# Optimization experiments

Hardware: AMD Instinct MI355X
Metric: run time of the kernel (lower is better)

## Reference

```python
import jax, jax.numpy as jnp
import numpy as np

B, T, D, H = 256, 128, 76, 128  # batch, time, features, lstm hidden (bidirectional -> 2H states)


def setup_inputs() -> dict:
    key = jax.random.key(0)
    ks = jax.random.split(key, 30)
    u = lambda k, shape: jax.random.uniform(k, shape, jnp.float32, -0.1, 0.1)
    inp = {}
    inp['x'] = jax.random.normal(ks[0], (B, T, D), jnp.float32)
    inp['eps_z'] = jax.random.normal(ks[1], (2, B, H), jnp.float32)
    inp['eps_on'] = jax.random.normal(ks[2], (B, T, 2 * H), jnp.float32)
    # encoder/decoder bidirectional LSTM weights: [dir, 4H, in] / [dir, 4H, H] / [dir, 4H]
    inp['enc_Wih'] = u(ks[3], (2, 4 * H, D)); inp['enc_Whh'] = u(ks[4], (2, 4 * H, H)); inp['enc_b'] = u(ks[5], (2, 4 * H))
    inp['dec_Wih'] = u(ks[6], (2, 4 * H, D)); inp['dec_Whh'] = u(ks[7], (2, 4 * H, H)); inp['dec_b'] = u(ks[8], (2, 4 * H))
    inp['Wzmu'] = u(ks[9], (H, H)); inp['bzmu'] = u(ks[10], (H,))
    inp['Wzlv'] = u(ks[11], (H, H)); inp['bzlv'] = u(ks[12], (H,))
    inp['Womu'] = u(ks[13], (2 * H, 2 * H)); inp['bomu'] = u(ks[14], (2 * H,))
    inp['Wolv'] = u(ks[15], (2 * H, 2 * H)); inp['bolv'] = u(ks[16], (2 * H,))
    inp['att_v'] = u(ks[17], (2 * H,))
    inp['att_W1'] = u(ks[18], (2 * H, 2 * H)); inp['att_b1'] = u(ks[19], (2 * H,))
    inp['att_W2'] = u(ks[20], (2 * H, 2 * H)); inp['att_b2'] = u(ks[21], (2 * H,))
    inp['Wout'] = u(ks[22], (D, 4 * H)); inp['bout'] = u(ks[23], (D,))
    return inp


def lstm_cell(xt, h, c, Wih, Whh, b):
    # PyTorch gate order: i, f, g, o
    g = xt @ Wih.T + h @ Whh.T + b
    i, f, gg, o = jnp.split(g, 4, axis=-1)
    c = jax.nn.sigmoid(f) * c + jax.nn.sigmoid(i) * jnp.tanh(gg)
    h = jax.nn.sigmoid(o) * jnp.tanh(c)
    return h, c


def reference(x, eps_z, eps_on, enc_Wih, enc_Whh, enc_b, dec_Wih, dec_Whh, dec_b,
              Wzmu, bzmu, Wzlv, bzlv, Womu, bomu, Wolv, bolv,
              att_v, att_W1, att_b1, att_W2, att_b2, Wout, bout):
    Bx, Tx, Dx = x.shape
    Hx = enc_Whh.shape[-1]
    xT = jnp.swapaxes(x, 0, 1)  # [T,B,D]
    h0 = jnp.zeros((Bx, Hx), x.dtype)
    c0 = jnp.zeros((Bx, Hx), x.dtype)

    def enc_step(d):
        def step(carry, xt):
            h, c = carry
            h, c = lstm_cell(xt, h, c, enc_Wih[d], enc_Whh[d], enc_b[d])
            return (h, c), h
        return step

    (hf, _), out_f = jax.lax.scan(enc_step(0), (h0, c0), xT)
    (hb, _), out_b = jax.lax.scan(enc_step(1), (h0, c0), xT[::-1])
    on = jnp.swapaxes(jnp.concatenate([out_f, out_b[::-1]], axis=-1), 0, 1)  # [B,T,2H]
    hn = jnp.stack([hf, hb])  # [2,B,H]

    # VAE reparameterization on final hidden and on encoder outputs
    mu_z = hn @ Wzmu.T + bzmu
    logvar_z = hn @ Wzlv.T + bzlv
    z = mu_z + eps_z * jnp.exp(0.5 * logvar_z)  # [2,B,H]
    mu_on = on @ Womu.T + bomu
    logvar_on = on @ Wolv.T + bolv
    on_s = mu_on + eps_on * jnp.exp(0.5 * logvar_on)  # [B,T,2H]

    # attention key projection precomputed once (W_2(values))
    W2v = on_s @ att_W2.T + att_b2  # [B,T,2H]
    # teacher forcing (prob=1.0): step t input is zeros at t=0, x[:,t-1] after
    dec_in = jnp.concatenate([jnp.zeros((1, Bx, Dx), x.dtype), xT[:-1]], axis=0)  # [T,B,D]

    def dec_step(carry, inp_t):
        h, c = carry  # each [2,B,H]
        q = jnp.concatenate([h[0], h[1]], axis=1)  # [B,2H]
        scores = jnp.tanh((q @ att_W1.T + att_b1)[:, None, :] + W2v) @ att_v  # [B,T]
        w = jax.nn.softmax(scores, axis=1)
        # (weights.unsqueeze(2) * values).mean(dim=1) -> weighted sum / T
        ctx = jnp.einsum('bt,btd->bd', w, on_s) / Tx  # [B,2H]
        h0n, c0n = lstm_cell(inp_t, h[0], c[0], dec_Wih[0], dec_Whh[0], dec_b[0])
        h1n, c1n = lstm_cell(inp_t, h[1], c[1], dec_Wih[1], dec_Whh[1], dec_b[1])
        out = jnp.concatenate([h0n, h1n, ctx], axis=1) @ Wout.T + bout  # [B,D]
        return (jnp.stack([h0n, h1n]), jnp.stack([c0n, c1n])), out

    _, outs = jax.lax.scan(dec_step, (z, jnp.zeros((2, Bx, Hx), x.dtype)), dec_in)
    return jnp.swapaxes(outs, 0, 1)  # [B,T,D] reconstruction
```

## Files before the change

kernel.cpp:

```cpp
#include <hip/hip_runtime.h>
#include <hip/hip_fp16.h>

#define B 256
#define T 128
#define D 76
#define H 128
#define G 512
#define H2 256

typedef unsigned int uint32;
typedef unsigned short ushort16;
typedef _Float16 h2_t __attribute__((ext_vector_type(2)));
typedef _Float16 f16x8 __attribute__((ext_vector_type(8)));
typedef float f32x4 __attribute__((ext_vector_type(4)));

__device__ __forceinline__ float sigm(float x){ return 1.0f/(1.0f+__expf(-x)); }
__device__ __forceinline__ float fast_rcp(float x){ float r; asm volatile("v_rcp_f32 %0, %1" : "=v"(r) : "v"(x)); return r; }
__device__ __forceinline__ float fast_tanh(float x){ return 1.0f - 2.0f*fast_rcp(1.0f + __expf(2.0f*x)); }
__device__ __forceinline__ ushort16 f2bf(float f){ uint32 u=__float_as_uint(f); return (ushort16)((u + 0x7fffu + ((u>>16)&1u))>>16); }
__device__ __forceinline__ uint32 pk_f16(float a, float b){
  return (uint32)__half_as_ushort(__float2half(a)) | ((uint32)__half_as_ushort(__float2half(b))<<16);
}
__device__ __forceinline__ float dot2(uint32 w, uint32 h, float acc){
  return __builtin_amdgcn_fdot2(__builtin_bit_cast(h2_t, w), __builtin_bit_cast(h2_t, h), acc, false);
}
__device__ __forceinline__ f32x4 mfma16(uint4 a, uint4 b, f32x4 c){
  return __builtin_amdgcn_mfma_f32_16x16x32_f16(
    __builtin_bit_cast(f16x8, a), __builtin_bit_cast(f16x8, b), c, 0, 0, 0);
}

struct PrepArgs {
  const float* src[2];
  float* dst[2];
  int R[2]; int C[2];
};
__global__ __launch_bounds__(256) void prep_k(PrepArgs a){
  int seg = blockIdx.x >> 5;
  const float* s=a.src[seg]; float* d=a.dst[seg];
  int R=a.R[seg], C=a.C[seg], tot=R*C;
  for (int i=(blockIdx.x&31)*256+threadIdx.x; i<tot; i+=32*256){
    int r=i/C, c=i-r*C;
    d[(size_t)c*R + r] = s[i];
  }
}

struct Pack2Args { const float* src[9]; uint32* dst[9]; int N[9]; int K[9]; };
__global__ __launch_bounds__(256) void pack2_k(Pack2Args a){
  int seg = blockIdx.x >> 5;
  const float* s=a.src[seg]; uint32* d=a.dst[seg];
  int N=a.N[seg], K=a.K[seg], tot=N*(K>>1);
  for (int i=(blockIdx.x&31)*256+threadIdx.x; i<tot; i+=32*256){
    int k2=i/N, j=i-k2*N;
    float2 w = *(const float2*)(s + (size_t)j*K + 2*k2);
    d[(size_t)k2*N + j] = pk_f16(w.x, w.y);
  }
}

__global__ __launch_bounds__(256) void pack_whh_k(
  const float* __restrict__ eWhh, const float* __restrict__ dWhh,
  uint32* __restrict__ wpkE, uint32* __restrict__ wpkD)
{
  int idx = blockIdx.x*256 + threadIdx.x;
  int phase = idx >> 16;
  int rem = idx & 65535;
  int d = rem >> 15;
  int k2 = (rem >> 9) & 63;
  int jc = rem & 511;
  int gate = (jc>>4)&3;
  int cell = (jc&15) + 16*(jc>>6);
  int jsrc = gate*128 + cell;
  const float* Wsrc = phase ? dWhh : eWhh;
  float2 wa = *(const float2*)(Wsrc + ((size_t)(d*512 + jsrc))*128 + 2*k2);
  (phase ? wpkD : wpkE)[rem] = pk_f16(wa.x, wa.y);
}

__global__ __launch_bounds__(256) void xg_k(
  const float* __restrict__ x, const uint32* __restrict__ wx, const float* __restrict__ bias,
  __half* __restrict__ xgh, int shift)
{
  int d = blockIdx.x >> 11;
  int blk = blockIdx.x & 2047;
  int b = blk >> 3, t0 = (blk & 7) * 16;
  int tid = threadIdx.x;
  __shared__ __align__(16) uint32 xs[16][40];
  for (int i=tid;i<16*38;i+=256){
    int r=i/38, k2=i-r*38, ts=t0+r-shift;
    float2 xv = (ts>=0) ? *(const float2*)(x + ((size_t)b*T+ts)*D + 2*k2) : make_float2(0.f,0.f);
    xs[r][k2] = pk_f16(xv.x, xv.y);
  }
  __syncthreads();
  const uint32* W = wx + (size_t)d*38*512;
  float a0[16], a1[16];
  #pragma unroll
  for(int r=0;r<16;r++){a0[r]=0.f;a1[r]=0.f;}
  #pragma unroll
  for (int k8=0;k8<9;k8++){
    int k2=4*k8;
    uint32 w00=W[(size_t)(k2+0)*512+tid], w01=W[(size_t)(k2+0)*512+tid+256];
    uint32 w10=W[(size_t)(k2+1)*512+tid], w11=W[(size_t)(k2+1)*512+tid+256];
    uint32 w20=W[(size_t)(k2+2)*512+tid], w21=W[(size_t)(k2+2)*512+tid+256];
    uint32 w30=W[(size_t)(k2+3)*512+tid], w31=W[(size_t)(k2+3)*512+tid+256];
    #pragma unroll
    for(int r=0;r<16;r++){
      uint4 u = *(const uint4*)&xs[r][k2];
      a0[r]=dot2(u.x,w00,a0[r]); a0[r]=dot2(u.y,w10,a0[r]);
      a0[r]=dot2(u.z,w20,a0[r]); a0[r]=dot2(u.w,w30,a0[r]);
      a1[r]=dot2(u.x,w01,a1[r]); a1[r]=dot2(u.y,w11,a1[r]);
      a1[r]=dot2(u.z,w21,a1[r]); a1[r]=dot2(u.w,w31,a1[r]);
    }
  }
  {
    uint32 w00=W[(size_t)36*512+tid], w01=W[(size_t)36*512+tid+256];
    uint32 w10=W[(size_t)37*512+tid], w11=W[(size_t)37*512+tid+256];
    #pragma unroll
    for(int r=0;r<16;r++){
      uint2 u = *(const uint2*)&xs[r][36];
      a0[r]=dot2(u.x,w00,a0[r]); a0[r]=dot2(u.y,w10,a0[r]);
      a1[r]=dot2(u.x,w01,a1[r]); a1[r]=dot2(u.y,w11,a1[r]);
    }
  }
  float bb0=bias[d*G+tid], bb1=bias[d*G+tid+256];
  #pragma unroll
  for(int r=0;r<16;r++){
    size_t row = (size_t)(d*B + b)*T + (t0+r);
    xgh[row*512 + tid]       = __float2half(a0[r]+bb0);
    xgh[row*512 + tid + 256] = __float2half(a1[r]+bb1);
  }
}

template<int ENC>
__global__ __launch_bounds__(512,2) void rec_k(
  const __half* __restrict__ xgh, const uint32* __restrict__ wpk,
  const __half* __restrict__ h16r, __half* __restrict__ on16,
  float* __restrict__ h_fin, uint32* __restrict__ h16w)
{
  int d = blockIdx.x >> 8;
  int b = blockIdx.x & 255;
  int tid = threadIdx.x;
  int lane = tid & 63;
  int gate = lane >> 4;
  int cell = (lane & 15) + 16*(tid >> 6);
  int jmap = gate*128 + cell;
  __shared__ __align__(16) __half hsd[2][H];
  uint32 wreg[64];
  const uint32* wp = wpk + (size_t)d*64*512;
  #pragma unroll
  for (int k2=0;k2<64;k2++) wreg[k2] = wp[k2*512 + tid];
  if (tid < H){
    if (ENC) hsd[0][tid] = __float2half(0.f);
    else     hsd[0][tid] = h16r[((size_t)d*B + b)*H + tid];
  }
  float creg = 0.f, hlast = 0.f;
  const __half* xrow = xgh + (size_t)(d*B + b)*T*512;
  int te0 = ENC ? (d ? (T-1) : 0) : 0;
  __half xr_next = xrow[(size_t)te0*512 + jmap];
  __syncthreads();
  int p = 0;
  for (int t=0;t<T;t++){
    int te = ENC ? (d ? (T-1-t) : t) : t;
    __half xr = xr_next;
    if (t+1 < T){
      int tn = ENC ? (d ? (T-2-t) : (t+1)) : (t+1);
      xr_next = xrow[(size_t)tn*512 + jmap];
    }
    const uint4* h128 = (const uint4*)hsd[p];
    float acc0 = 0.f, acc1 = 0.f;
    #pragma unroll
    for (int k8=0;k8<16;k8++){
      uint4 hv4 = h128[k8];
      acc0 = dot2(wreg[4*k8+0], hv4.x, acc0);
      acc1 = dot2(wreg[4*k8+1], hv4.y, acc1);
      acc0 = dot2(wreg[4*k8+2], hv4.z, acc0);
      acc1 = dot2(wreg[4*k8+3], hv4.w, acc1);
    }
    float gpre = acc0 + acc1 + __half2float(xr);
    float kmul = (gate==2) ? 2.f : 1.f;
    float s = sigm(kmul*gpre);
    float act = (gate==2) ? fmaf(2.f, s, -1.f) : s;
    int src = lane & 15;
    float f_ = __shfl(act, src+16, 64);
    float g_ = __shfl(act, src+32, 64);
    float o_ = __shfl(act, src+48, 64);
    if (gate==0){
      creg = f_*creg + act*g_;
      float hv = o_*fast_tanh(creg);
      hlast = hv;
      hsd[p^1][cell] = __float2half(hv);
      if (ENC){
        on16[((size_t)b*T + te)*H2 + d*H + cell] = __float2half(hv);
      } else {
        float nb = __shfl_xor(hv, 1);
        if ((cell&1)==0)
          h16w[(((size_t)(t+1)*2 + d)*B + b)*64 + (cell>>1)] = pk_f16(hv, nb);
      }
    }
    __syncthreads();
    p ^= 1;
  }
  if (ENC && gate==0) h_fin[(size_t)d*B*H + (size_t)b*H + cell] = hlast;
}

__global__ __launch_bounds__(128) void z_k(
  const float* __restrict__ h_fin, const float* __restrict__ WzmuT, const float* __restrict__ bzmu,
  const float* __restrict__ WzlvT, const float* __restrict__ bzlv, const float* __restrict__ eps_z,
  uint32* __restrict__ h16w)
{
  __shared__ float hr[H];
  int d = blockIdx.x >> 8; int b = blockIdx.x & 255;
  int j = threadIdx.x;
  hr[j] = h_fin[(size_t)d*B*H + (size_t)b*H + j];
  __syncthreads();
  float mu=bzmu[j], lv=bzlv[j];
  #pragma unroll 4
  for(int k=0;k<H;k++){ float hv=hr[k]; mu+=hv*WzmuT[k*H+j]; lv+=hv*WzlvT[k*H+j]; }
  float z = mu + eps_z[(size_t)d*B*H + (size_t)b*H + j]*__expf(0.5f*lv);
  float nb = __shfl_xor(z, 1);
  if ((j&1)==0)
    h16w[(((size_t)0*2 + d)*B + b)*64 + (j>>1)] = pk_f16(z, nb);
}

__global__ __launch_bounds__(256) void onsw2v_k(
  const uint32* __restrict__ on32, const uint32* __restrict__ wpmu, const float* __restrict__ bomu,
  const uint32* __restrict__ wplv, const float* __restrict__ bolv, const float* __restrict__ eps_on,
  const uint32* __restrict__ wp2, const float* __restrict__ b2,
  uint32* __restrict__ onsT, float* __restrict__ ebg)
{
  __shared__ __align__(16) uint32 tl[32][128];
  __shared__ __align__(16) uint32 t2p[32][128];
  size_t row0=(size_t)blockIdx.x*32;
  int b = (int)(row0 >> 7), t0 = (int)(row0 & 127);
  int tid=threadIdx.x;
  int wv = tid>>6, lane = tid&63;
  int n0 = wv*64;
  int lr = lane & 15, kq = lane >> 4;
  for(int i=tid;i<32*128;i+=256) ((uint32*)tl)[i] = on32[row0*128 + i];
  __syncthreads();
  f32x4 accM[2][4], accL[2][4];
  #pragma unroll
  for (int mt=0;mt<2;mt++)
    #pragma unroll
    for (int nt=0;nt<4;nt++){ accM[mt][nt]=(f32x4){0,0,0,0}; accL[mt][nt]=(f32x4){0,0,0,0}; }
  for (int kb=0;kb<8;kb++){
    int k2b = kb*16 + kq*4;
    uint4 aA0 = *(const uint4*)&tl[lr][k2b];
    uint4 aA1 = *(const uint4*)&tl[16+lr][k2b];
    #pragma unroll
    for (int nt=0;nt<4;nt++){
      int n = n0 + nt*16 + lr;
      uint4 bM, bL;
      bM.x = wpmu[(size_t)(k2b+0)*H2 + n]; bM.y = wpmu[(size_t)(k2b+1)*H2 + n];
      bM.z = wpmu[(size_t)(k2b+2)*H2 + n]; bM.w = wpmu[(size_t)(k2b+3)*H2 + n];
      bL.x = wplv[(size_t)(k2b+0)*H2 + n]; bL.y = wplv[(size_t)(k2b+1)*H2 + n];
      bL.z = wplv[(size_t)(k2b+2)*H2 + n]; bL.w = wplv[(size_t)(k2b+3)*H2 + n];
      accM[0][nt] = mfma16(aA0, bM, accM[0][nt]);
      accM[1][nt] = mfma16(aA1, bM, accM[1][nt]);
      accL[0][nt] = mfma16(aA0, bL, accL[0][nt]);
      accL[1][nt] = mfma16(aA1, bL, accL[1][nt]);
    }
  }
  #pragma unroll
  for (int mt=0;mt<2;mt++){
    #pragma unroll
    for (int nt=0;nt<4;nt++){
      int col = n0 + nt*16 + lr;
      float bm = bomu[col], bl = bolv[col];
      #pragma unroll
      for (int r=0;r<4;r++){
        int rl = mt*16 + kq*4 + r;
        size_t rowg = row0 + rl;
        float mu = accM[mt][nt][r] + bm;
        float lv = accL[mt][nt][r] + bl;
        float v = mu + eps_on[rowg*H2 + col]*__expf(0.5f*lv);
        float nb = __shfl_xor(v, 1);
        if ((lr&1)==0) t2p[rl][col>>1] = pk_f16(v, nb);
      }
    }
  }
  __syncthreads();
  #pragma unroll
  for(int rr=0;rr<16;rr++){
    uint32 ua = t2p[2*rr][tid>>1], ub = t2p[2*rr+1][tid>>1];
    uint32 ha = (tid&1) ? (ua>>16) : (ua & 0xffffu);
    uint32 hb = (tid&1) ? (ub>>16) : (ub & 0xffffu);
    onsT[((size_t)b*H2 + tid)*64 + (t0>>1) + rr] = ha | (hb<<16);
  }
  f32x4 acc3[2][4];
  #pragma unroll
  for (int mt=0;mt<2;mt++)
    #pragma unroll
    for (int nt=0;nt<4;nt++) acc3[mt][nt]=(f32x4){0,0,0,0};
  for (int kb=0;kb<8;kb++){
    int k2b = kb*16 + kq*4;
    uint4 aA0 = *(const uint4*)&t2p[lr][k2b];
    uint4 aA1 = *(const uint4*)&t2p[16+lr][k2b];
    #pragma unroll
    for (int nt=0;nt<4;nt++){
      int n = n0 + nt*16 + lr;
      uint4 bW;
      bW.x = wp2[(size_t)(k2b+0)*H2 + n]; bW.y = wp2[(size_t)(k2b+1)*H2 + n];
      bW.z = wp2[(size_t)(k2b+2)*H2 + n]; bW.w = wp2[(size_t)(k2b+3)*H2 + n];
      acc3[0][nt] = mfma16(aA0, bW, acc3[0][nt]);
      acc3[1][nt] = mfma16(aA1, bW, acc3[1][nt]);
    }
  }
  #pragma unroll
  for (int mt=0;mt<2;mt++){
    #pragma unroll
    for (int nt=0;nt<4;nt++){
      int col = n0 + nt*16 + lr;
      float bb = b2[col];
      #pragma unroll
      for (int r=0;r<4;r++){
        int rl = mt*16 + kq*4 + r;
        ebg[(row0 + rl)*H2 + col] = __expf(2.0f*(acc3[mt][nt][r] + bb));
      }
    }
  }
}

__global__ __launch_bounds__(256) void qp_all_k(
  const uint32* __restrict__ h16, const uint32* __restrict__ wp1, const float* __restrict__ b1,
  float* __restrict__ eqg)
{
  int m0 = blockIdx.x*32; int b = m0>>7; int t0 = m0&127;
  __shared__ __align__(16) uint32 tile[32][128];
  int tid=threadIdx.x;
  int wv = tid>>6, lane = tid&63;
  int n0 = wv*64;
  int lr = lane & 15, kq = lane >> 4;
  for (int i=tid;i<32*128;i+=256){
    int r=i>>7, c=i&127; int dd=c>>6, kk2=c&63;
    tile[r][c] = h16[(((size_t)(t0+r)*2 + dd)*B + b)*64 + kk2];
  }
  __syncthreads();
  f32x4 acc[2][4];
  #pragma unroll
  for (int mt=0;mt<2;mt++)
    #pragma unroll
    for (int nt=0;nt<4;nt++) acc[mt][nt]=(f32x4){0,0,0,0};
  for (int kb=0;kb<8;kb++){
    int k2b = kb*16 + kq*4;
    uint4 aA0 = *(const uint4*)&tile[lr][k2b];
    uint4 aA1 = *(const uint4*)&tile[16+lr][k2b];
    #pragma unroll
    for (int nt=0;nt<4;nt++){
      int n = n0 + nt*16 + lr;
      uint4 bW;
      bW.x = wp1[(size_t)(k2b+0)*H2 + n]; bW.y = wp1[(size_t)(k2b+1)*H2 + n];
      bW.z = wp1[(size_t)(k2b+2)*H2 + n]; bW.w = wp1[(size_t)(k2b+3)*H2 + n];
      acc[0][nt] = mfma16(aA0, bW, acc[0][nt]);
      acc[1][nt] = mfma16(aA1, bW, acc[1][nt]);
    }
  }
  #pragma unroll
  for (int mt=0;mt<2;mt++){
    #pragma unroll
    for (int nt=0;nt<4;nt++){
      int col = n0 + nt*16 + lr;
      float bb = b1[col];
      #pragma unroll
      for (int r=0;r<4;r++){
        int rl = mt*16 + kq*4 + r;
        eqg[(size_t)(m0 + rl)*H2 + col] = __expf(2.0f*(acc[mt][nt][r] + bb));
      }
    }
  }
}

__global__ __launch_bounds__(512,2) void score_k(
  const float* __restrict__ eqg, const float* __restrict__ ebg,
  const float* __restrict__ att_v, uint32* __restrict__ sc16)
{
  int b  = blockIdx.x >> 1;
  int t0 = (blockIdx.x & 1) * 64;
  int tid = threadIdx.x;
  int jq = tid & 15, ttb = tid >> 4;
  __shared__ __align__(16) float eqs[2][4*320];
  __shared__ __align__(16) float scl[2][4][T];
  __shared__ float wsum8[2][8];
  __shared__ __align__(16) float wvsp[320];
  float eb0[16], eb1[16], eb2[16], eb3[16];
  float vsum_mine = 0.f;
  {
    const float* ebb = ebg + (size_t)b*T*H2;
    #pragma unroll
    for (int ii=0;ii<16;ii++){
      int j = 16*jq + ii;
      eb0[ii] = ebb[(size_t)(ttb    )*H2 + j];
      eb1[ii] = ebb[(size_t)(ttb+32 )*H2 + j];
      eb2[ii] = ebb[(size_t)(ttb+64 )*H2 + j];
      eb3[ii] = ebb[(size_t)(ttb+96 )*H2 + j];
      vsum_mine += att_v[j];
    }
  }
  if (tid < H2) wvsp[(tid>>4)*20 + (tid&15)] = -2.0f*att_v[tid];
  if (tid < 256){
    int q = tid>>6, l = 4*(tid&63);
    float4 v = ((const float4*)(eqg + ((size_t)b*T + t0 + q)*H2))[tid&63];
    *(float4*)&eqs[0][q*320 + (l>>4)*20 + (l&15)] = v;
  }
  __syncthreads();
  int buf = 0;
  for (int tq=0; tq<64; tq+=4){
    int cur = (tq>>2)&1;
    if (tq+4 < 64 && tid < 256){
      int q = tid>>6, l = 4*(tid&63);
      float4 v = ((const float4*)(eqg + ((size_t)b*T + t0+tq+4 + q)*H2))[tid&63];
      *(float4*)&eqs[buf^1][q*320 + (l>>4)*20 + (l&15)] = v;
    }
    const float* eqb = eqs[buf];
    float a00=vsum_mine,a01=vsum_mine,a02=vsum_mine,a03=vsum_mine;
    float a10=vsum_mine,a11=vsum_mine,a12=vsum_mine,a13=vsum_mine;
    float a20=vsum_mine,a21=vsum_mine,a22=vsum_mine,a23=vsum_mine;
    float a30=vsum_mine,a31=vsum_mine,a32=vsum_mine,a33=vsum_mine;
    #pragma unroll
    for (int ii4=0; ii4<4; ii4++){
      float4 q0 = *(const float4*)&eqb[        jq*20 + 4*ii4];
      float4 q1 = *(const float4*)&eqb[320   + jq*20 + 4*ii4];
      float4 q2 = *(const float4*)&eqb[2*320 + jq*20 + 4*ii4];
      float4 q3 = *(const float4*)&eqb[3*320 + jq*20 + 4*ii4];
      float4 w4 = *(const float4*)&wvsp[jq*20 + 4*ii4];
      #pragma unroll
      for (int c=0;c<4;c++){
        int ii = 4*ii4 + c;
        float e0=eb0[ii], e1=eb1[ii], e2=eb2[ii], e3=eb3[ii];
        float q0c = (c==0)?q0.x:(c==1)?q0.y:(c==2)?q0.z:q0.w;
        float q1c = (c==0)?q1.x:(c==1)?q1.y:(c==2)?q1.z:q1.w;
        float q2c = (c==0)?q2.x:(c==1)?q2.y:(c==2)?q2.z:q2.w;
        float q3c = (c==0)?q3.x:(c==1)?q3.y:(c==2)?q3.z:q3.w;
        float w   = (c==0)?w4.x:(c==1)?w4.y:(c==2)?w4.z:w4.w;
        a00 = fmaf(w, fast_rcp(fmaf(e0,q0c,1.f)), a00);
        a01 = fmaf(w, fast_rcp(fmaf(e1,q0c,1.f)), a01);
        a02 = fmaf(w, fast_rcp(fmaf(e2,q0c,1.f)), a02);
        a03 = fmaf(w, fast_rcp(fmaf(e3,q0c,1.f)), a03);
        a10 = fmaf(w, fast_rcp(fmaf(e0,q1c,1.f)), a10);
        a11 = fmaf(w, fast_rcp(fmaf(e1,q1c,1.f)), a11);
        a12 = fmaf(w, fast_rcp(fmaf(e2,q1c,1.f)), a12);
        a13 = fmaf(w, fast_rcp(fmaf(e3,q1c,1.f)), a13);
        a20 = fmaf(w, fast_rcp(fmaf(e0,q2c,1.f)), a20);
        a21 = fmaf(w, fast_rcp(fmaf(e1,q2c,1.f)), a21);
        a22 = fmaf(w, fast_rcp(fmaf(e2,q2c,1.f)), a22);
        a23 = fmaf(w, fast_rcp(fmaf(e3,q2c,1.f)), a23);
        a30 = fmaf(w, fast_rcp(fmaf(e0,q3c,1.f)), a30);
        a31 = fmaf(w, fast_rcp(fmaf(e1,q3c,1.f)), a31);
        a32 = fmaf(w, fast_rcp(fmaf(e2,q3c,1.f)), a32);
        a33 = fmaf(w, fast_rcp(fmaf(e3,q3c,1.f)), a33);
      }
    }
    #pragma unroll
    for (int off=1; off<16; off<<=1){
      a00 += __shfl_xor(a00,off); a01 += __shfl_xor(a01,off);
      a02 += __shfl_xor(a02,off); a03 += __shfl_xor(a03,off);
      a10 += __shfl_xor(a10,off); a11 += __shfl_xor(a11,off);
      a12 += __shfl_xor(a12,off); a13 += __shfl_xor(a13,off);
      a20 += __shfl_xor(a20,off); a21 += __shfl_xor(a21,off);
      a22 += __shfl_xor(a22,off); a23 += __shfl_xor(a23,off);
      a30 += __shfl_xor(a30,off); a31 += __shfl_xor(a31,off);
      a32 += __shfl_xor(a32,off); a33 += __shfl_xor(a33,off);
    }
    if (jq==0){
      scl[cur][0][ttb]=__expf(a00); scl[cur][0][ttb+32]=__expf(a01);
      scl[cur][0][ttb+64]=__expf(a02); scl[cur][0][ttb+96]=__expf(a03);
      scl[cur][1][ttb]=__expf(a10); scl[cur][1][ttb+32]=__expf(a11);
      scl[cur][1][ttb+64]=__expf(a12); scl[cur][1][ttb+96]=__expf(a13);
      scl[cur][2][ttb]=__expf(a20); scl[cur][2][ttb+32]=__expf(a21);
      scl[cur][2][ttb+64]=__expf(a22); scl[cur][2][ttb+96]=__expf(a23);
      scl[cur][3][ttb]=__expf(a30); scl[cur][3][ttb+32]=__expf(a31);
      scl[cur][3][ttb+64]=__expf(a32); scl[cur][3][ttb+96]=__expf(a33);
    }
    __syncthreads();
    {
      int row = tid>>7;
      float e = scl[cur][row][tid&127];
      #pragma unroll
      for (int off=1; off<64; off<<=1) e += __shfl_xor(e,off);
      if ((tid&63)==0) wsum8[cur][tid>>6]=e;
    }
    __syncthreads();
    if (tid < 256){
      int row = tid>>6, i = tid&63;
      float tot = wsum8[cur][row*2] + wsum8[cur][row*2+1];
      float inv = fast_rcp(tot*128.0f);
      sc16[((size_t)b*T + t0+tq+row)*64 + i] =
        pk_f16(scl[cur][row][2*i]*inv, scl[cur][row][2*i+1]*inv);
    }
    buf ^= 1;
  }
}

__global__ __launch_bounds__(256,2) void pvout_k(
  const uint32* __restrict__ sc16, const uint32* __restrict__ onsT,
  const uint32* __restrict__ h16, const uint32* __restrict__ wpout,
  const float* __restrict__ bout, float* __restrict__ out)
{
  int b  = blockIdx.x >> 3;
  int t0 = (blockIdx.x & 7) * 16;
  int m0 = blockIdx.x*16;
  int tid = threadIdx.x;
  __shared__ uint32 scs[16][64];
  __shared__ __align__(16) uint32 rb[16][256];
  uint4 vreg[16];
  {
    const uint4* vp = (const uint4*)(onsT + ((size_t)b*H2 + tid)*64);
    #pragma unroll
    for (int k=0;k<16;k++) vreg[k] = vp[k];
  }
  for (int i=tid;i<1024;i+=256) ((uint32*)scs)[i] = sc16[((size_t)b*T + t0)*64 + i];
  for (int i=tid;i<16*128;i+=256){
    int r=i>>7, c=i&127;
    int t = t0+r;
    rb[r][c] = (c<64) ? h16[(((size_t)(t+1)*2 + 0)*B + b)*64 + c]
                      : h16[(((size_t)(t+1)*2 + 1)*B + b)*64 + (c-64)];
  }
  __syncthreads();
  for (int qt=0; qt<16; qt++){
    float a0=0.f,a1=0.f,a2=0.f,a3=0.f;
    #pragma unroll
    for (int k=0;k<16;k++){
      a0 = dot2(scs[qt][4*k+0], vreg[k].x, a0);
      a1 = dot2(scs[qt][4*k+1], vreg[k].y, a1);
      a2 = dot2(scs[qt][4*k+2], vreg[k].z, a2);
      a3 = dot2(scs[qt][4*k+3], vreg[k].w, a3);
    }
    float mine = (a0+a1)+(a2+a3);
    float nb = __shfl_xor(mine, 1);
    if ((tid&1)==0) rb[qt][128 + (tid>>1)] = pk_f16(mine, nb);
  }
  __syncthreads();
  for (int o=tid;o<16*D;o+=256){
    int r=o/D, j=o-r*D;
    float acc=bout[j];
    for (int k4=0;k4<64;k4++){
      uint4 u = *(const uint4*)&rb[r][4*k4];
      acc = dot2(u.x, wpout[(size_t)(4*k4+0)*D+j], acc);
      acc = dot2(u.y, wpout[(size_t)(4*k4+1)*D+j], acc);
      acc = dot2(u.z, wpout[(size_t)(4*k4+2)*D+j], acc);
      acc = dot2(u.w, wpout[(size_t)(4*k4+3)*D+j], acc);
    }
    out[((size_t)(m0+r))*D + j]=acc;
  }
}

extern "C" void kernel_launch(void* const* d_in, const int* in_sizes, int n_in,
                              void* d_out, int out_size, void* d_ws, size_t ws_size,
                              hipStream_t stream) {
  const float* x      =(const float*)d_in[0];
  const float* eps_z  =(const float*)d_in[1];
  const float* eps_on =(const float*)d_in[2];
  const float* enc_Wih=(const float*)d_in[3];
  const float* enc_Whh=(const float*)d_in[4];
  const float* enc_b  =(const float*)d_in[5];
  const float* dec_Wih=(const float*)d_in[6];
  const float* dec_Whh=(const float*)d_in[7];
  const float* dec_b  =(const float*)d_in[8];
  const float* Wzmu=(const float*)d_in[9];  const float* bzmu=(const float*)d_in[10];
  const float* Wzlv=(const float*)d_in[11]; const float* bzlv=(const float*)d_in[12];
  const float* Womu=(const float*)d_in[13]; const float* bomu=(const float*)d_in[14];
  const float* Wolv=(const float*)d_in[15]; const float* bolv=(const float*)d_in[16];
  const float* att_v=(const float*)d_in[17];
  const float* att_W1=(const float*)d_in[18]; const float* att_b1=(const float*)d_in[19];
  const float* att_W2=(const float*)d_in[20]; const float* att_b2=(const float*)d_in[21];
  const float* Wout=(const float*)d_in[22];  const float* bout=(const float*)d_in[23];
  float* out=(float*)d_out;
  float* ws=(float*)d_ws;
  (void)ws_size; (void)n_in; (void)in_sizes; (void)out_size;

  size_t o=0;
  float* WzmuT=ws+o; o+=H*H;
  float* WzlvT=ws+o; o+=H*H;
  uint32* wpkE=(uint32*)(ws+o); o+=65536;
  uint32* wpkD=(uint32*)(ws+o); o+=65536;
  uint32* wpmu=(uint32*)(ws+o); o+=32768;
  uint32* wplv=(uint32*)(ws+o); o+=32768;
  uint32* wp1 =(uint32*)(ws+o); o+=32768;
  uint32* wp2 =(uint32*)(ws+o); o+=32768;
  uint32* wpout=(uint32*)(ws+o); o+=19456;
  uint32* wxE =(uint32*)(ws+o); o+=38912;
  uint32* wxD =(uint32*)(ws+o); o+=38912;
  float* h_fin=ws+o; o+=2*B*H;
  __half* on16=(__half*)(ws+o); o+=(size_t)B*T*H2/2;
  uint32* h16 =(uint32*)(ws+o); o+=(size_t)(T+1)*2*B*64;
  float* Abase=ws+o; o+=16777216;
  float* Cbase=ws+o; o+=14680064;

  __half* xgh = (__half*)Abase;
  float* eqg  = Abase;
  uint32* onsT = (uint32*)Cbase;
  float* ebg  = Cbase + 4194304;
  uint32* sc16 = (uint32*)(Cbase + 4194304 + 8388608);

  PrepArgs pa;
  {
    const float* srcs[2]={Wzmu,Wzlv};
    float* dsts[2]={WzmuT,WzlvT};
    for(int i=0;i<2;i++){pa.src[i]=srcs[i];pa.dst[i]=dsts[i];pa.R[i]=H;pa.C[i]=H;}
  }
  Pack2Args p2;
  {
    const float* srcs[9]={Womu,Wolv,att_W1,att_W2,Wout,
                          enc_Wih, enc_Wih + (size_t)512*76,
                          dec_Wih, dec_Wih + (size_t)512*76};
    uint32* dsts[9]={wpmu,wplv,wp1,wp2,wpout, wxE, wxE+19456, wxD, wxD+19456};
    int Ns[9]={H2,H2,H2,H2,D, 512,512,512,512};
    int Ks[9]={H2,H2,H2,H2,G, D,D,D,D};
    for(int i=0;i<9;i++){p2.src[i]=srcs[i];p2.dst[i]=dsts[i];p2.N[i]=Ns[i];p2.K[i]=Ks[i];}
  }
  prep_k<<<64,256,0,stream>>>(pa);
  pack2_k<<<288,256,0,stream>>>(p2);
  pack_whh_k<<<512,256,0,stream>>>(enc_Whh, dec_Whh, wpkE, wpkD);

  xg_k<<<4096,256,0,stream>>>(x, wxE, enc_b, xgh, 0);
  rec_k<1><<<512,512,0,stream>>>(xgh, wpkE, nullptr, on16, h_fin, nullptr);
  z_k<<<512,128,0,stream>>>(h_fin, WzmuT,bzmu,WzlvT,bzlv,eps_z, h16);
  onsw2v_k<<<1024,256,0,stream>>>((const uint32*)on16,wpmu,bomu,wplv,bolv,eps_on,wp2,att_b2,onsT,ebg);

  xg_k<<<4096,256,0,stream>>>(x, wxD, dec_b, xgh, 1);
  rec_k<0><<<512,512,0,stream>>>(xgh, wpkD, (const __half*)h16, nullptr, nullptr, h16);

  qp_all_k<<<1024,256,0,stream>>>(h16, wp1, att_b1, eqg);
  score_k<<<512,512,0,stream>>>(eqg, ebg, att_v, sc16);
  pvout_k<<<2048,256,0,stream>>>(sc16, onsT, h16, wpout, bout, out);
}
```

Measured before the change: 698.5 us.

## Use MFMA for input-gate projection and pvout matmuls with padded weight packing

Replaces the scalar fdot2 GEMMs in xg_k (input-to-gate projection) and pvout_k (attention context plus output projection) with 16x16x32 f16 MFMA tiles. Weight packing now pads K and N to MFMA-friendly multiples (K to 96, output N to 80) with zeros. xg_k handles 32 rows per block with half the grid and writes packed half2 outputs. The aim is to cut ALU time in these non-recurrent GEMMs. In exchange there are more global weight loads per tile and shuffles in the epilogue.

```diff
diff --git a/kernel.cpp b/kernel.cpp
--- a/kernel.cpp
+++ b/kernel.cpp
@@ -17,7 +17,6 @@
 __device__ __forceinline__ float sigm(float x){ return 1.0f/(1.0f+__expf(-x)); }
 __device__ __forceinline__ float fast_rcp(float x){ float r; asm volatile("v_rcp_f32 %0, %1" : "=v"(r) : "v"(x)); return r; }
 __device__ __forceinline__ float fast_tanh(float x){ return 1.0f - 2.0f*fast_rcp(1.0f + __expf(2.0f*x)); }
-__device__ __forceinline__ ushort16 f2bf(float f){ uint32 u=__float_as_uint(f); return (ushort16)((u + 0x7fffu + ((u>>16)&1u))>>16); }
 __device__ __forceinline__ uint32 pk_f16(float a, float b){
   return (uint32)__half_as_ushort(__float2half(a)) | ((uint32)__half_as_ushort(__float2half(b))<<16);
 }
@@ -44,15 +43,20 @@
   }
 }
 
-struct Pack2Args { const float* src[9]; uint32* dst[9]; int N[9]; int K[9]; };
+struct Pack2Args { const float* src[9]; uint32* dst[9]; int N[9]; int NP[9]; int K[9]; int KP2[9]; };
 __global__ __launch_bounds__(256) void pack2_k(Pack2Args a){
   int seg = blockIdx.x >> 5;
   const float* s=a.src[seg]; uint32* d=a.dst[seg];
-  int N=a.N[seg], K=a.K[seg], tot=N*(K>>1);
+  int N=a.N[seg], NP=a.NP[seg], K=a.K[seg], KP2=a.KP2[seg];
+  int tot=NP*KP2;
   for (int i=(blockIdx.x&31)*256+threadIdx.x; i<tot; i+=32*256){
-    int k2=i/N, j=i-k2*N;
-    float2 w = *(const float2*)(s + (size_t)j*K + 2*k2);
-    d[(size_t)k2*N + j] = pk_f16(w.x, w.y);
+    int k2=i/NP, j=i-k2*NP;
+    uint32 v = 0;
+    if (j < N && 2*k2 < K){
+      float2 w = *(const float2*)(s + (size_t)j*K + 2*k2);
+      v = pk_f16(w.x, w.y);
+    }
+    d[(size_t)k2*NP + j] = v;
   }
 }
 
@@ -76,55 +80,60 @@
 
 __global__ __launch_bounds__(256) void xg_k(
   const float* __restrict__ x, const uint32* __restrict__ wx, const float* __restrict__ bias,
-  __half* __restrict__ xgh, int shift)
-{
-  int d = blockIdx.x >> 11;
-  int blk = blockIdx.x & 2047;
-  int b = blk >> 3, t0 = (blk & 7) * 16;
+  uint32* __restrict__ xgp, int shift)
+{
+  int m0 = blockIdx.x*32;
+  int d = m0 >> 15;
+  int rem = m0 & 32767;
+  int b = rem >> 7, t0 = rem & 127;
   int tid = threadIdx.x;
-  __shared__ __align__(16) uint32 xs[16][40];
-  for (int i=tid;i<16*38;i+=256){
-    int r=i/38, k2=i-r*38, ts=t0+r-shift;
-    float2 xv = (ts>=0) ? *(const float2*)(x + ((size_t)b*T+ts)*D + 2*k2) : make_float2(0.f,0.f);
+  int wv = tid>>6, lane = tid&63;
+  int n0 = wv*128;
+  int lr = lane & 15, kq = lane >> 4;
+  __shared__ __align__(16) uint32 xs[32][48];
+  for (int i=tid;i<32*48;i+=256){
+    int r=i/48, k2=i-r*48, ts=t0+r-shift;
+    float2 xv = (k2<38 && ts>=0) ? *(const float2*)(x + ((size_t)b*T+ts)*D + 2*k2)
+                                 : make_float2(0.f,0.f);
     xs[r][k2] = pk_f16(xv.x, xv.y);
   }
   __syncthreads();
-  const uint32* W = wx + (size_t)d*38*512;
-  float a0[16], a1[16];
-  #pragma unroll
-  for(int r=0;r<16;r++){a0[r]=0.f;a1[r]=0.f;}
-  #pragma unroll
-  for (int k8=0;k8<9;k8++){
-    int k2=4*k8;
-    uint32 w00=W[(size_t)(k2+0)*512+tid], w01=W[(size_t)(k2+0)*512+tid+256];
-    uint32 w10=W[(size_t)(k2+1)*512+tid], w11=W[(size_t)(k2+1)*512+tid+256];
-    uint32 w20=W[(size_t)(k2+2)*512+tid], w21=W[(size_t)(k2+2)*512+tid+256];
-    uint32 w30=W[(size_t)(k2+3)*512+tid], w31=W[(size_t)(k2+3)*512+tid+256];
-    #pragma unroll
-    for(int r=0;r<16;r++){
-      uint4 u = *(const uint4*)&xs[r][k2];
-      a0[r]=dot2(u.x,w00,a0[r]); a0[r]=dot2(u.y,w10,a0[r]);
-      a0[r]=dot2(u.z,w20,a0[r]); a0[r]=dot2(u.w,w30,a0[r]);
-      a1[r]=dot2(u.x,w01,a1[r]); a1[r]=dot2(u.y,w11,a1[r]);
-      a1[r]=dot2(u.z,w21,a1[r]); a1[r]=dot2(u.w,w31,a1[r]);
-    }
-  }
-  {
-    uint32 w00=W[(size_t)36*512+tid], w01=W[(size_t)36*512+tid+256];
-    uint32 w10=W[(size_t)37*512+tid], w11=W[(size_t)37*512+tid+256];
-    #pragma unroll
-    for(int r=0;r<16;r++){
-      uint2 u = *(const uint2*)&xs[r][36];
-      a0[r]=dot2(u.x,w00,a0[r]); a0[r]=dot2(u.y,w10,a0[r]);
-      a1[r]=dot2(u.x,w01,a1[r]); a1[r]=dot2(u.y,w11,a1[r]);
-    }
-  }
-  float bb0=bias[d*G+tid], bb1=bias[d*G+tid+256];
-  #pragma unroll
-  for(int r=0;r<16;r++){
-    size_t row = (size_t)(d*B + b)*T + (t0+r);
-    xgh[row*512 + tid]       = __float2half(a0[r]+bb0);
-    xgh[row*512 + tid + 256] = __float2half(a1[r]+bb1);
+  const uint32* W = wx + (size_t)d*48*512;
+  f32x4 acc[2][8];
+  #pragma unroll
+  for (int mt=0;mt<2;mt++)
+    #pragma unroll
+    for (int nt=0;nt<8;nt++) acc[mt][nt]=(f32x4){0,0,0,0};
+  #pragma unroll
+  for (int kb=0;kb<3;kb++){
+    int k2b = kb*16 + kq*4;
+    uint4 a0 = *(const uint4*)&xs[lr][k2b];
+    uint4 a1 = *(const uint4*)&xs[16+lr][k2b];
+    #pragma unroll
+    for (int nt=0;nt<8;nt++){
+      int n = n0 + nt*16 + lr;
+      uint4 bw;
+      bw.x = W[(size_t)(k2b+0)*512 + n]; bw.y = W[(size_t)(k2b+1)*512 + n];
+      bw.z = W[(size_t)(k2b+2)*512 + n]; bw.w = W[(size_t)(k2b+3)*512 + n];
+      acc[0][nt] = mfma16(a0, bw, acc[0][nt]);
+      acc[1][nt] = mfma16(a1, bw, acc[1][nt]);
+    }
+  }
+  #pragma unroll
+  for (int mt=0;mt<2;mt++){
+    #pragma unroll
+    for (int nt=0;nt<8;nt++){
+      int col = n0 + nt*16 + lr;
+      float bb = bias[d*G + col];
+      #pragma unroll
+      for (int r=0;r<4;r++){
+        int rl = mt*16 + kq*4 + r;
+        float v = acc[mt][nt][r] + bb;
+        float nb = __shfl_xor(v, 1);
+        if ((lr&1)==0)
+          xgp[((size_t)(m0+rl)*512 + col)>>1] = pk_f16(v, nb);
+      }
+    }
   }
 }
 
@@ -497,14 +506,10 @@
   int t0 = (blockIdx.x & 7) * 16;
   int m0 = blockIdx.x*16;
   int tid = threadIdx.x;
-  __shared__ uint32 scs[16][64];
+  int wv = tid>>6, lane = tid&63;
+  int lr = lane & 15, kq = lane >> 4;
+  __shared__ __align__(16) uint32 scs[16][64];
   __shared__ __align__(16) uint32 rb[16][256];
-  uint4 vreg[16];
-  {
-    const uint4* vp = (const uint4*)(onsT + ((size_t)b*H2 + tid)*64);
-    #pragma unroll
-    for (int k=0;k<16;k++) vreg[k] = vp[k];
-  }
   for (int i=tid;i<1024;i+=256) ((uint32*)scs)[i] = sc16[((size_t)b*T + t0)*64 + i];
   for (int i=tid;i<16*128;i+=256){
     int r=i>>7, c=i&127;
@@ -513,31 +518,53 @@
                       : h16[(((size_t)(t+1)*2 + 1)*B + b)*64 + (c-64)];
   }
   __syncthreads();
-  for (int qt=0; qt<16; qt++){
-    float a0=0.f,a1=0.f,a2=0.f,a3=0.f;
-    #pragma unroll
-    for (int k=0;k<16;k++){
-      a0 = dot2(scs[qt][4*k+0], vreg[k].x, a0);
-      a1 = dot2(scs[qt][4*k+1], vreg[k].y, a1);
-      a2 = dot2(scs[qt][4*k+2], vreg[k].z, a2);
-      a3 = dot2(scs[qt][4*k+3], vreg[k].w, a3);
-    }
-    float mine = (a0+a1)+(a2+a3);
-    float nb = __shfl_xor(mine, 1);
-    if ((tid&1)==0) rb[qt][128 + (tid>>1)] = pk_f16(mine, nb);
-  }
-  __syncthreads();
-  for (int o=tid;o<16*D;o+=256){
-    int r=o/D, j=o-r*D;
-    float acc=bout[j];
-    for (int k4=0;k4<64;k4++){
-      uint4 u = *(const uint4*)&rb[r][4*k4];
-      acc = dot2(u.x, wpout[(size_t)(4*k4+0)*D+j], acc);
-      acc = dot2(u.y, wpout[(size_t)(4*k4+1)*D+j], acc);
-      acc = dot2(u.z, wpout[(size_t)(4*k4+2)*D+j], acc);
-      acc = dot2(u.w, wpout[(size_t)(4*k4+3)*D+j], acc);
-    }
-    out[((size_t)(m0+r))*D + j]=acc;
+  {
+    int n0 = wv*64;
+    f32x4 accP[4];
+    #pragma unroll
+    for (int nt=0;nt<4;nt++) accP[nt]=(f32x4){0,0,0,0};
+    #pragma unroll
+    for (int kb=0;kb<4;kb++){
+      int k2b = kb*16 + kq*4;
+      uint4 a = *(const uint4*)&scs[lr][k2b];
+      #pragma unroll
+      for (int nt=0;nt<4;nt++){
+        int j = n0 + nt*16 + lr;
+        uint4 bw = *(const uint4*)(onsT + ((size_t)b*H2 + j)*64 + k2b);
+        accP[nt] = mfma16(a, bw, accP[nt]);
+      }
+    }
+    #pragma unroll
+    for (int nt=0;nt<4;nt++){
+      int j = n0 + nt*16 + lr;
+      #pragma unroll
+      for (int r=0;r<4;r++){
+        int row = kq*4 + r;
+        float v = accP[nt][r];
+        float nb = __shfl_xor(v, 1);
+        if ((lr&1)==0) rb[row][128 + (j>>1)] = pk_f16(v, nb);
+      }
+    }
+  }
+  __syncthreads();
+  for (int tt=wv; tt<5; tt+=4){
+    f32x4 acc = (f32x4){0,0,0,0};
+    #pragma unroll
+    for (int kb=0;kb<16;kb++){
+      int k2b = kb*16 + kq*4;
+      uint4 a = *(const uint4*)&rb[lr][k2b];
+      uint4 bw;
+      bw.x = wpout[(size_t)(k2b+0)*80 + tt*16+lr]; bw.y = wpout[(size_t)(k2b+1)*80 + tt*16+lr];
+      bw.z = wpout[(size_t)(k2b+2)*80 + tt*16+lr]; bw.w = wpout[(size_t)(k2b+3)*80 + tt*16+lr];
+      acc = mfma16(a, bw, acc);
+    }
+    int col = tt*16 + lr;
+    if (col < D){
+      float bb = bout[col];
+      #pragma unroll
+      for (int r=0;r<4;r++)
+        out[(size_t)(m0 + kq*4 + r)*D + col] = acc[r] + bb;
+    }
   }
 }
 
@@ -574,15 +601,16 @@
   uint32* wplv=(uint32*)(ws+o); o+=32768;
   uint32* wp1 =(uint32*)(ws+o); o+=32768;
   uint32* wp2 =(uint32*)(ws+o); o+=32768;
-  uint32* wpout=(uint32*)(ws+o); o+=19456;
-  uint32* wxE =(uint32*)(ws+o); o+=38912;
-  uint32* wxD =(uint32*)(ws+o); o+=38912;
+  uint32* wpout=(uint32*)(ws+o); o+=20480;
+  uint32* wxE =(uint32*)(ws+o); o+=49152;
+  uint32* wxD =(uint32*)(ws+o); o+=49152;
   float* h_fin=ws+o; o+=2*B*H;
   __half* on16=(__half*)(ws+o); o+=(size_t)B*T*H2/2;
   uint32* h16 =(uint32*)(ws+o); o+=(size_t)(T+1)*2*B*64;
   float* Abase=ws+o; o+=16777216;
   float* Cbase=ws+o; o+=14680064;
 
+  uint32* xgp = (uint32*)Abase;
   __half* xgh = (__half*)Abase;
   float* eqg  = Abase;
   uint32* onsT = (uint32*)Cbase;
@@ -600,21 +628,23 @@
     const float* srcs[9]={Womu,Wolv,att_W1,att_W2,Wout,
                           enc_Wih, enc_Wih + (size_t)512*76,
                           dec_Wih, dec_Wih + (size_t)512*76};
-    uint32* dsts[9]={wpmu,wplv,wp1,wp2,wpout, wxE, wxE+19456, wxD, wxD+19456};
-    int Ns[9]={H2,H2,H2,H2,D, 512,512,512,512};
-    int Ks[9]={H2,H2,H2,H2,G, D,D,D,D};
-    for(int i=0;i<9;i++){p2.src[i]=srcs[i];p2.dst[i]=dsts[i];p2.N[i]=Ns[i];p2.K[i]=Ks[i];}
+    uint32* dsts[9]={wpmu,wplv,wp1,wp2,wpout, wxE, wxE+24576, wxD, wxD+24576};
+    int Ns [9]={H2,H2,H2,H2, D, 512,512,512,512};
+    int NPs[9]={H2,H2,H2,H2, 80, 512,512,512,512};
+    int Ks [9]={H2,H2,H2,H2, G, D,D,D,D};
+    int KP2[9]={128,128,128,128, 256, 48,48,48,48};
+    for(int i=0;i<9;i++){p2.src[i]=srcs[i];p2.dst[i]=dsts[i];p2.N[i]=Ns[i];p2.NP[i]=NPs[i];p2.K[i]=Ks[i];p2.KP2[i]=KP2[i];}
   }
   prep_k<<<64,256,0,stream>>>(pa);
   pack2_k<<<288,256,0,stream>>>(p2);
   pack_whh_k<<<512,256,0,stream>>>(enc_Whh, dec_Whh, wpkE, wpkD);
 
-  xg_k<<<4096,256,0,stream>>>(x, wxE, enc_b, xgh, 0);
+  xg_k<<<2048,256,0,stream>>>(x, wxE, enc_b, xgp, 0);
   rec_k<1><<<512,512,0,stream>>>(xgh, wpkE, nullptr, on16, h_fin, nullptr);
   z_k<<<512,128,0,stream>>>(h_fin, WzmuT,bzmu,WzlvT,bzlv,eps_z, h16);
   onsw2v_k<<<1024,256,0,stream>>>((const uint32*)on16,wpmu,bomu,wplv,bolv,eps_on,wp2,att_b2,onsT,ebg);
 
-  xg_k<<<4096,256,0,stream>>>(x, wxD, dec_b, xgh, 1);
+  xg_k<<<2048,256,0,stream>>>(x, wxD, dec_b, xgp, 1);
   rec_k<0><<<512,512,0,stream>>>(xgh, wpkD, (const __half*)h16, nullptr, nullptr, h16);
 
   qp_all_k<<<1024,256,0,stream>>>(h16, wp1, att_b1, eqg);
```

Result: faster. 612.3 us (-12.3%).
